# Optimization experiments

Measured on AMD Instinct MI355X. Metric: run time of the kernel, lower is better.

The kernel has to match this reference:

```python
import jax, jax.numpy as jnp
import numpy as np

N = 100000      # atoms
P = 6400000     # pairs (~64 neighbors/atom)
T = 16          # atom types
BOX_L = 30.0    # cubic box edge (Angstrom)


def setup_inputs() -> dict:
    key = jax.random.key(0)
    k_c, k_i, k_off, k_a, k_b, k_t = jax.random.split(key, 6)
    coords = jax.random.uniform(k_c, (N, 3), dtype=jnp.float32) * BOX_L
    # build pairs with i != j so distances are never exactly zero
    i = jax.random.randint(k_i, (P,), 0, N)
    off = jax.random.randint(k_off, (P,), 1, N)
    j = (i + off) % N
    pairs = jnp.stack([i, j], axis=1).astype(jnp.int64)
    box = (BOX_L * jnp.eye(3)).astype(jnp.float32)
    A = jax.random.uniform(k_a, (T, T), dtype=jnp.float32)
    B = jax.random.uniform(k_b, (T, T), dtype=jnp.float32) + 0.5
    atom_types = jax.random.randint(k_t, (N,), 0, T).astype(jnp.int64)
    return {
        "coords": coords,
        "pairs": pairs,
        "box": box,
        "A": A,
        "B": B,
        "cutoff": 12,
        "atom_types": atom_types,
    }


def reference(coords, pairs, box, A, B, cutoff, atom_types):
    # gather pair endpoints: (P,3)
    dr = coords[pairs[:, 1]] - coords[pairs[:, 0]]
    # minimum-image convention (general triclinic box): fractional wrap
    inv_box = jnp.linalg.inv(box)
    s = dr @ inv_box
    s = s - jnp.round(s)
    dr_vecs = s @ box
    r = jnp.linalg.norm(dr_vecs, axis=1)          # (P,)
    # type-pair indexed amplitudes / inverse lengths
    ti = atom_types[pairs[:, 0]]
    tj = atom_types[pairs[:, 1]]
    A_ij = A[ti, tj]
    B_ij = B[ti, tj]
    # Slater energy: x = B r, Pfac = x^2/3 + x + 1, E = A * Pfac * exp(-x)
    x = B_ij * r
    Pfac = x * x / 3.0 + x + 1.0
    ene = A_ij * Pfac * jnp.exp(-x)
    ene = jnp.where(r <= jnp.float32(cutoff), ene, 0.0)
    return jnp.sum(ene)
```

## Files before the change

### kernel.cpp

```cpp
#include <hip/hip_runtime.h>


#ifndef SLATER_T
#define SLATER_T 16
#endif

typedef int  vint4  __attribute__((ext_vector_type(4)));

__global__ __launch_bounds__(256)
void repack_kernel(const float* __restrict__ coords,
                   const int* __restrict__ types,
                   float4* __restrict__ packed,
                   float* __restrict__ out, int out_size,
                   int n)
{
    int i = blockIdx.x * blockDim.x + threadIdx.x;
    if (i < out_size) out[i] = 0.0f;
    int stride = gridDim.x * blockDim.x;
    for (; i < n; i += stride) {
        float4 v;
        v.x = coords[3 * i + 0];
        v.y = coords[3 * i + 1];
        v.z = coords[3 * i + 2];
        v.w = __int_as_float(types[i]);
        packed[i] = v;
    }
}

__global__ __launch_bounds__(256)
void zero_kernel(float* __restrict__ out, int out_size)
{
    int i = blockIdx.x * blockDim.x + threadIdx.x;
    if (i < out_size) out[i] = 0.0f;
}

template <bool PACKED>
__global__ __launch_bounds__(256)
void slater_kernel(const int* __restrict__ pairs,
                   const float4* __restrict__ packed,
                   const float* __restrict__ coords,
                   const int* __restrict__ types,
                   const float* __restrict__ A,
                   const float* __restrict__ B,
                   const float* __restrict__ box,
                   const int* __restrict__ cutoffp,
                   float* __restrict__ out,
                   int nP)
{
    __shared__ float2 tab[SLATER_T * SLATER_T];
    if (threadIdx.x < SLATER_T * SLATER_T)
        tab[threadIdx.x] = make_float2(A[threadIdx.x], B[threadIdx.x]);
    __syncthreads();

    float b00 = box[0], b01 = box[1], b02 = box[2];
    float b10 = box[3], b11 = box[4], b12 = box[5];
    float b20 = box[6], b21 = box[7], b22 = box[8];

    float C00 =  (b11 * b22 - b12 * b21);
    float C01 = -(b10 * b22 - b12 * b20);
    float C02 =  (b10 * b21 - b11 * b20);
    float C10 = -(b01 * b22 - b02 * b21);
    float C11 =  (b00 * b22 - b02 * b20);
    float C12 = -(b00 * b21 - b01 * b20);
    float C20 =  (b01 * b12 - b02 * b11);
    float C21 = -(b00 * b12 - b02 * b10);
    float C22 =  (b00 * b11 - b01 * b10);
    float det = b00 * C00 + b01 * C01 + b02 * C02;
    float inv_det = 1.0f / det;
    float i00 = C00 * inv_det, i01 = C10 * inv_det, i02 = C20 * inv_det;
    float i10 = C01 * inv_det, i11 = C11 * inv_det, i12 = C21 * inv_det;
    float i20 = C02 * inv_det, i21 = C12 * inv_det, i22 = C22 * inv_det;

    float cut = (float)(*cutoffp);

    float acc = 0.0f;
    int tid    = blockIdx.x * blockDim.x + threadIdx.x;
    int stride = gridDim.x * blockDim.x;

    auto fetch = [&](int idx) -> float4 {
        if (PACKED) {
            return packed[idx];
        } else {
            float4 v;
            v.x = coords[3 * idx + 0];
            v.y = coords[3 * idx + 1];
            v.z = coords[3 * idx + 2];
            v.w = __int_as_float(types[idx]);
            return v;
        }
    };

    auto body = [&](float4 ca, float4 cb) {
        int ti = __float_as_int(ca.w);
        int tj = __float_as_int(cb.w);
        float2 ab = tab[ti * SLATER_T + tj];

        float dx = cb.x - ca.x, dy = cb.y - ca.y, dz = cb.z - ca.z;

        float s0 = dx * i00 + dy * i10 + dz * i20;
        float s1 = dx * i01 + dy * i11 + dz * i21;
        float s2 = dx * i02 + dy * i12 + dz * i22;
        s0 -= rintf(s0);
        s1 -= rintf(s1);
        s2 -= rintf(s2);
        float d0 = s0 * b00 + s1 * b10 + s2 * b20;
        float d1 = s0 * b01 + s1 * b11 + s2 * b21;
        float d2 = s0 * b02 + s1 * b12 + s2 * b22;

        float r = sqrtf(d0 * d0 + d1 * d1 + d2 * d2);
        float x  = ab.y * r;
        float pf = x * x * (1.0f / 3.0f) + x + 1.0f;
        float e  = ab.x * pf * __expf(-x);
        acc += (r <= cut) ? e : 0.0f;
    };

    const vint4* p4 = (const vint4*)pairs;
    int n4 = nP >> 1;
    const int step = stride * 2;

    int i0 = tid;
    for (; i0 + stride < n4; i0 += step) {
        vint4 pa = __builtin_nontemporal_load(p4 + i0);
        vint4 pb = __builtin_nontemporal_load(p4 + i0 + stride);
        float4 c0 = fetch(pa.x);
        float4 c1 = fetch(pa.y);
        float4 c2 = fetch(pa.z);
        float4 c3 = fetch(pa.w);
        float4 c4 = fetch(pb.x);
        float4 c5 = fetch(pb.y);
        float4 c6 = fetch(pb.z);
        float4 c7 = fetch(pb.w);
        body(c0, c1);
        body(c2, c3);
        body(c4, c5);
        body(c6, c7);
    }
    if (i0 < n4) {
        vint4 pa = __builtin_nontemporal_load(p4 + i0);
        float4 c0 = fetch(pa.x);
        float4 c1 = fetch(pa.y);
        float4 c2 = fetch(pa.z);
        float4 c3 = fetch(pa.w);
        body(c0, c1);
        body(c2, c3);
    }
    if (tid == 0 && (nP & 1)) {
        int ia = pairs[2 * (nP - 1)], ja = pairs[2 * (nP - 1) + 1];
        body(fetch(ia), fetch(ja));
    }

    #pragma unroll
    for (int off = 32; off > 0; off >>= 1)
        acc += __shfl_down(acc, off, 64);

    __shared__ float wsum[4];
    int lane = threadIdx.x & 63;
    int wid  = threadIdx.x >> 6;
    if (lane == 0) wsum[wid] = acc;
    __syncthreads();
    if (threadIdx.x == 0) {
        float s = wsum[0] + wsum[1] + wsum[2] + wsum[3];
        atomicAdd(out, s);
    }
}

extern "C" void kernel_launch(void* const* d_in, const int* in_sizes, int n_in,
                              void* d_out, int out_size, void* d_ws, size_t ws_size,
                              hipStream_t stream)
{
    const float* coords = (const float*)d_in[0];
    const int*   pairs  = (const int*)d_in[1];
    const float* box    = (const float*)d_in[2];
    const float* A      = (const float*)d_in[3];
    const float* B      = (const float*)d_in[4];
    const int*   cutoff = (const int*)d_in[5];
    const int*   types  = (const int*)d_in[6];

    int n  = in_sizes[0] / 3;
    int nP = in_sizes[1] / 2;

    float* out = (float*)d_out;

    size_t need = (size_t)n * sizeof(float4);

    const int THREADS = 256;
    const int BLOCKS  = 2048;

    if (ws_size >= need) {
        float4* packed = (float4*)d_ws;
        int rblocks = (n + THREADS - 1) / THREADS;
        if (rblocks > 2048) rblocks = 2048;
        repack_kernel<<<rblocks, THREADS, 0, stream>>>(coords, types, packed,
                                                       out, out_size, n);
        slater_kernel<true><<<BLOCKS, THREADS, 0, stream>>>(
            pairs, packed, nullptr, nullptr, A, B,
            box, cutoff, out, nP);
    } else {
        zero_kernel<<<(out_size + THREADS - 1) / THREADS, THREADS, 0, stream>>>(out, out_size);
        slater_kernel<false><<<BLOCKS, THREADS, 0, stream>>>(
            pairs, nullptr, coords, types, A, B,
            box, cutoff, out, nP);
    }
}
```

Baseline: 72.44 us.

## Software-pipeline pair index and coordinate gathers across loop iterations

Restructures the packed Slater kernel into a rotating pipeline. Pair indices are prefetched two iterations ahead and the gathered coordinates one iteration ahead, and a scheduling barrier keeps those loads ahead of the arithmetic. This is meant to hide gather latency behind the energy math, at the cost of more registers and predicated dummy loads. The grid is also cut from 2048 to 1536 blocks, and the unpacked fallback path becomes a plain per-pair kernel.

```diff
diff --git a/kernel.cpp b/kernel.cpp
--- a/kernel.cpp
+++ b/kernel.cpp
@@ -5,7 +5,7 @@
 #define SLATER_T 16
 #endif
 
-typedef int  vint4  __attribute__((ext_vector_type(4)));
+typedef int vint4 __attribute__((ext_vector_type(4)));
 
 __global__ __launch_bounds__(256)
 void repack_kernel(const float* __restrict__ coords,
@@ -34,18 +34,15 @@
     if (i < out_size) out[i] = 0.0f;
 }
 
-template <bool PACKED>
-__global__ __launch_bounds__(256)
-void slater_kernel(const int* __restrict__ pairs,
-                   const float4* __restrict__ packed,
-                   const float* __restrict__ coords,
-                   const int* __restrict__ types,
-                   const float* __restrict__ A,
-                   const float* __restrict__ B,
-                   const float* __restrict__ box,
-                   const int* __restrict__ cutoffp,
-                   float* __restrict__ out,
-                   int nP)
+__global__ __launch_bounds__(256)
+void slater_pipe(const int* __restrict__ pairs,
+                 const float4* __restrict__ packed,
+                 const float* __restrict__ A,
+                 const float* __restrict__ B,
+                 const float* __restrict__ box,
+                 const int* __restrict__ cutoffp,
+                 float* __restrict__ out,
+                 int nP)
 {
     __shared__ float2 tab[SLATER_T * SLATER_T];
     if (threadIdx.x < SLATER_T * SLATER_T)
@@ -76,27 +73,18 @@
     float acc = 0.0f;
     int tid    = blockIdx.x * blockDim.x + threadIdx.x;
     int stride = gridDim.x * blockDim.x;
-
-    auto fetch = [&](int idx) -> float4 {
-        if (PACKED) {
-            return packed[idx];
-        } else {
-            float4 v;
-            v.x = coords[3 * idx + 0];
-            v.y = coords[3 * idx + 1];
-            v.z = coords[3 * idx + 2];
-            v.w = __int_as_float(types[idx]);
-            return v;
-        }
+    const vint4* p4 = (const vint4*)pairs;
+    int n4   = nP >> 1;
+    int step = stride * 2;
+
+    auto ld4 = [&](int idx, bool v) -> vint4 {
+        return __builtin_nontemporal_load(p4 + (v ? idx : 0));
     };
-
-    auto body = [&](float4 ca, float4 cb) {
+    auto body = [&](float4 ca, float4 cb, bool val) {
         int ti = __float_as_int(ca.w);
         int tj = __float_as_int(cb.w);
         float2 ab = tab[ti * SLATER_T + tj];
-
         float dx = cb.x - ca.x, dy = cb.y - ca.y, dz = cb.z - ca.z;
-
         float s0 = dx * i00 + dy * i10 + dz * i20;
         float s1 = dx * i01 + dy * i11 + dz * i21;
         float s2 = dx * i02 + dy * i12 + dz * i22;
@@ -106,62 +94,138 @@
         float d0 = s0 * b00 + s1 * b10 + s2 * b20;
         float d1 = s0 * b01 + s1 * b11 + s2 * b21;
         float d2 = s0 * b02 + s1 * b12 + s2 * b22;
-
+        float r = sqrtf(d0 * d0 + d1 * d1 + d2 * d2);
+        float x  = ab.y * r;
+        float pf = x * x * (1.0f / 3.0f) + x + 1.0f;
+        float e  = ab.x * pf * __expf(-x);
+        acc += (val && r <= cut) ? e : 0.0f;
+    };
+
+    int i0 = tid;
+    int i1 = tid + step;
+    bool a0 = i0 < n4,          b0 = (i0 + stride) < n4;
+    bool a1 = i1 < n4,          b1 = (i1 + stride) < n4;
+
+    vint4 pA = ld4(i0, a0),          pB = ld4(i0 + stride, b0);
+    vint4 qA = ld4(i1, a1),          qB = ld4(i1 + stride, b1);
+
+    float4 c0 = packed[pA.x], c1 = packed[pA.y], c2 = packed[pA.z], c3 = packed[pA.w];
+    float4 c4 = packed[pB.x], c5 = packed[pB.y], c6 = packed[pB.z], c7 = packed[pB.w];
+
+    while (a0) {
+        int i2 = i1 + step;
+        bool a2 = i2 < n4, b2 = (i2 + stride) < n4;
+        vint4 rA = ld4(i2, a2);
+        vint4 rB = ld4(i2 + stride, b2);
+
+        float4 m0, m1, m2, m3, m4, m5, m6, m7;
+        if (a1) { m0 = packed[qA.x]; m1 = packed[qA.y]; m2 = packed[qA.z]; m3 = packed[qA.w]; }
+        else    { m0 = m1 = m2 = m3 = make_float4(0.f, 0.f, 0.f, 0.f); }
+        if (b1) { m4 = packed[qB.x]; m5 = packed[qB.y]; m6 = packed[qB.z]; m7 = packed[qB.w]; }
+        else    { m4 = m5 = m6 = m7 = make_float4(0.f, 0.f, 0.f, 0.f); }
+        __builtin_amdgcn_sched_barrier(0);
+
+        body(c0, c1, a0);
+        body(c2, c3, a0);
+        body(c4, c5, b0);
+        body(c6, c7, b0);
+
+        c0 = m0; c1 = m1; c2 = m2; c3 = m3;
+        c4 = m4; c5 = m5; c6 = m6; c7 = m7;
+        qA = rA; qB = rB;
+        a0 = a1; b0 = b1; a1 = a2; b1 = b2;
+        i1 = i2;
+    }
+
+    if (tid == 0 && (nP & 1)) {
+        int ia = pairs[2 * (nP - 1)], ja = pairs[2 * (nP - 1) + 1];
+        body(packed[ia], packed[ja], true);
+    }
+
+    #pragma unroll
+    for (int off = 32; off > 0; off >>= 1)
+        acc += __shfl_down(acc, off, 64);
+
+    __shared__ float wsum[4];
+    int lane = threadIdx.x & 63;
+    int wid  = threadIdx.x >> 6;
+    if (lane == 0) wsum[wid] = acc;
+    __syncthreads();
+    if (threadIdx.x == 0) {
+        float s = wsum[0] + wsum[1] + wsum[2] + wsum[3];
+        atomicAdd(out, s);
+    }
+}
+
+__global__ __launch_bounds__(256)
+void slater_simple(const int* __restrict__ pairs,
+                   const float* __restrict__ coords,
+                   const int* __restrict__ types,
+                   const float* __restrict__ A,
+                   const float* __restrict__ B,
+                   const float* __restrict__ box,
+                   const int* __restrict__ cutoffp,
+                   float* __restrict__ out,
+                   int nP)
+{
+    __shared__ float2 tab[SLATER_T * SLATER_T];
+    if (threadIdx.x < SLATER_T * SLATER_T)
+        tab[threadIdx.x] = make_float2(A[threadIdx.x], B[threadIdx.x]);
+    __syncthreads();
+
+    float b00 = box[0], b01 = box[1], b02 = box[2];
+    float b10 = box[3], b11 = box[4], b12 = box[5];
+    float b20 = box[6], b21 = box[7], b22 = box[8];
+    float C00 =  (b11 * b22 - b12 * b21);
+    float C01 = -(b10 * b22 - b12 * b20);
+    float C02 =  (b10 * b21 - b11 * b20);
+    float C10 = -(b01 * b22 - b02 * b21);
+    float C11 =  (b00 * b22 - b02 * b20);
+    float C12 = -(b00 * b21 - b01 * b20);
+    float C20 =  (b01 * b12 - b02 * b11);
+    float C21 = -(b00 * b12 - b02 * b10);
+    float C22 =  (b00 * b11 - b01 * b10);
+    float det = b00 * C00 + b01 * C01 + b02 * C02;
+    float inv_det = 1.0f / det;
+    float i00 = C00 * inv_det, i01 = C10 * inv_det, i02 = C20 * inv_det;
+    float i10 = C01 * inv_det, i11 = C11 * inv_det, i12 = C21 * inv_det;
+    float i20 = C02 * inv_det, i21 = C12 * inv_det, i22 = C22 * inv_det;
+    float cut = (float)(*cutoffp);
+
+    float acc = 0.0f;
+    int tid    = blockIdx.x * blockDim.x + threadIdx.x;
+    int stride = gridDim.x * blockDim.x;
+    for (int p = tid; p < nP; p += stride) {
+        int ia = pairs[2 * p], ja = pairs[2 * p + 1];
+        float ax = coords[3 * ia], ay = coords[3 * ia + 1], az = coords[3 * ia + 2];
+        float bx = coords[3 * ja], by = coords[3 * ja + 1], bz = coords[3 * ja + 2];
+        int ti = types[ia], tj = types[ja];
+        float2 ab = tab[ti * SLATER_T + tj];
+        float dx = bx - ax, dy = by - ay, dz = bz - az;
+        float s0 = dx * i00 + dy * i10 + dz * i20;
+        float s1 = dx * i01 + dy * i11 + dz * i21;
+        float s2 = dx * i02 + dy * i12 + dz * i22;
+        s0 -= rintf(s0); s1 -= rintf(s1); s2 -= rintf(s2);
+        float d0 = s0 * b00 + s1 * b10 + s2 * b20;
+        float d1 = s0 * b01 + s1 * b11 + s2 * b21;
+        float d2 = s0 * b02 + s1 * b12 + s2 * b22;
         float r = sqrtf(d0 * d0 + d1 * d1 + d2 * d2);
         float x  = ab.y * r;
         float pf = x * x * (1.0f / 3.0f) + x + 1.0f;
         float e  = ab.x * pf * __expf(-x);
         acc += (r <= cut) ? e : 0.0f;
-    };
-
-    const vint4* p4 = (const vint4*)pairs;
-    int n4 = nP >> 1;
-    const int step = stride * 2;
-
-    int i0 = tid;
-    for (; i0 + stride < n4; i0 += step) {
-        vint4 pa = __builtin_nontemporal_load(p4 + i0);
-        vint4 pb = __builtin_nontemporal_load(p4 + i0 + stride);
-        float4 c0 = fetch(pa.x);
-        float4 c1 = fetch(pa.y);
-        float4 c2 = fetch(pa.z);
-        float4 c3 = fetch(pa.w);
-        float4 c4 = fetch(pb.x);
-        float4 c5 = fetch(pb.y);
-        float4 c6 = fetch(pb.z);
-        float4 c7 = fetch(pb.w);
-        body(c0, c1);
-        body(c2, c3);
-        body(c4, c5);
-        body(c6, c7);
-    }
-    if (i0 < n4) {
-        vint4 pa = __builtin_nontemporal_load(p4 + i0);
-        float4 c0 = fetch(pa.x);
-        float4 c1 = fetch(pa.y);
-        float4 c2 = fetch(pa.z);
-        float4 c3 = fetch(pa.w);
-        body(c0, c1);
-        body(c2, c3);
-    }
-    if (tid == 0 && (nP & 1)) {
-        int ia = pairs[2 * (nP - 1)], ja = pairs[2 * (nP - 1) + 1];
-        body(fetch(ia), fetch(ja));
     }
 
     #pragma unroll
     for (int off = 32; off > 0; off >>= 1)
         acc += __shfl_down(acc, off, 64);
-
     __shared__ float wsum[4];
     int lane = threadIdx.x & 63;
     int wid  = threadIdx.x >> 6;
     if (lane == 0) wsum[wid] = acc;
     __syncthreads();
-    if (threadIdx.x == 0) {
-        float s = wsum[0] + wsum[1] + wsum[2] + wsum[3];
-        atomicAdd(out, s);
-    }
+    if (threadIdx.x == 0)
+        atomicAdd(out, wsum[0] + wsum[1] + wsum[2] + wsum[3]);
 }
 
 extern "C" void kernel_launch(void* const* d_in, const int* in_sizes, int n_in,
@@ -184,7 +248,7 @@
     size_t need = (size_t)n * sizeof(float4);
 
     const int THREADS = 256;
-    const int BLOCKS  = 2048;
+    const int BLOCKS  = 1536;
 
     if (ws_size >= need) {
         float4* packed = (float4*)d_ws;
@@ -192,13 +256,11 @@
         if (rblocks > 2048) rblocks = 2048;
         repack_kernel<<<rblocks, THREADS, 0, stream>>>(coords, types, packed,
                                                        out, out_size, n);
-        slater_kernel<true><<<BLOCKS, THREADS, 0, stream>>>(
-            pairs, packed, nullptr, nullptr, A, B,
-            box, cutoff, out, nP);
+        slater_pipe<<<BLOCKS, THREADS, 0, stream>>>(pairs, packed, A, B,
+                                                    box, cutoff, out, nP);
     } else {
         zero_kernel<<<(out_size + THREADS - 1) / THREADS, THREADS, 0, stream>>>(out, out_size);
-        slater_kernel<false><<<BLOCKS, THREADS, 0, stream>>>(
-            pairs, nullptr, coords, types, A, B,
-            box, cutoff, out, nP);
-    }
-}
+        slater_simple<<<2048, THREADS, 0, stream>>>(pairs, coords, types, A, B,
+                                                    box, cutoff, out, nP);
+    }
+}
```

Result: faster. 70.06 us (-3.3%).
